# Optimization experiments

Measured on AMD Instinct MI355X. Metric: run time of the kernel, lower is better.

The kernel has to match this reference:

```python
import jax, jax.numpy as jnp
import numpy as np

D_MODEL = 2048
N_HEADS = 16
HEAD_DIM = D_MODEL // N_HEADS


def setup_inputs() -> dict:
    key = jax.random.key(0)
    ks = jax.random.split(key, 5)
    scale = 1.0 / np.sqrt(D_MODEL)
    x = jax.random.normal(ks[0], (2, 2048, D_MODEL), dtype=jnp.float32)
    W_qkv = jax.random.normal(ks[1], (D_MODEL, 3 * D_MODEL), dtype=jnp.float32) * scale
    b_qkv = jnp.zeros((3 * D_MODEL,), dtype=jnp.float32)
    W_out = jax.random.normal(ks[2], (D_MODEL, D_MODEL), dtype=jnp.float32) * scale
    b_out = jnp.zeros((D_MODEL,), dtype=jnp.float32)
    return {"x": x, "W_qkv": W_qkv, "b_qkv": b_qkv, "W_out": W_out, "b_out": b_out}


def reference(x, W_qkv, b_qkv, W_out, b_out):
    bsz, seq_len, _ = x.shape
    # QKV projection: (b, s, 3*d) -> (3, b, h, s, hd)
    qkv = x @ W_qkv + b_qkv
    qkv = qkv.reshape(bsz, seq_len, 3, N_HEADS, HEAD_DIM)
    qkv = jnp.transpose(qkv, (2, 0, 3, 1, 4))
    q, k, v = qkv[0], qkv[1], qkv[2]
    # scaled dot-product scores: (b, h, s, s)
    scores = jnp.einsum("bhqd,bhkd->bhqk", q, k) / np.sqrt(HEAD_DIM).astype(np.float32)
    causal = jnp.tril(jnp.ones((seq_len, seq_len), dtype=bool))
    scores = jnp.where(causal[None, None], scores, -jnp.inf)
    attn = jax.nn.softmax(scores, axis=-1)
    # attention output: (b, h, s, hd) -> (b, s, d)
    out = jnp.einsum("bhqk,bhkd->bhqd", attn, v)
    out = jnp.transpose(out, (0, 2, 1, 3)).reshape(bsz, seq_len, D_MODEL)
    y = out @ W_out + b_out
    return y
```

## Files before the change

kernel.cpp:

```cpp
#include <hip/hip_runtime.h>
#include <stdint.h>
#include <stddef.h>


typedef __attribute__((ext_vector_type(8))) short bf16x8;
typedef __attribute__((ext_vector_type(4))) float f32x4;

#define SOFT_SCALE 0.12751743075419806f

__device__ __forceinline__ short f2bf(float f) {
  union { float f; unsigned u; } v; v.f = f;
  unsigned u = v.u + 0x7fffu + ((v.u >> 16) & 1u);
  return (short)(u >> 16);
}

__device__ __forceinline__ void gload_lds16(const void* g, const void* l) {
  __builtin_amdgcn_global_load_lds(
      (__attribute__((address_space(1))) void*)(uintptr_t)g,
      (__attribute__((address_space(3))) void*)(uintptr_t)l,
      16, 0, 0);
}

__global__ __launch_bounds__(256) void cast_f32_bf16(
    const float* __restrict__ in, short* __restrict__ out, int n8) {
  int i = blockIdx.x * 256 + threadIdx.x;
  if (i >= n8) return;
  float4 a = ((const float4*)in)[i * 2];
  float4 b = ((const float4*)in)[i * 2 + 1];
  bf16x8 o;
  o[0] = f2bf(a.x); o[1] = f2bf(a.y); o[2] = f2bf(a.z); o[3] = f2bf(a.w);
  o[4] = f2bf(b.x); o[5] = f2bf(b.y); o[6] = f2bf(b.z); o[7] = f2bf(b.w);
  ((bf16x8*)out)[i] = o;
}

__global__ __launch_bounds__(256) void transpose_cast_w(
    const float* __restrict__ W, short* __restrict__ WT, int K, int N) {
  __shared__ short t[32][33];
  int k0 = blockIdx.x * 32, n0 = blockIdx.y * 32;
  int r = threadIdx.x >> 3;
  int c = (threadIdx.x & 7) * 4;
  float4 v = *(const float4*)(W + (size_t)(k0 + r) * N + n0 + c);
  t[r][c + 0] = f2bf(v.x); t[r][c + 1] = f2bf(v.y);
  t[r][c + 2] = f2bf(v.z); t[r][c + 3] = f2bf(v.w);
  __syncthreads();
  short4 o;
  o.x = t[c + 0][r]; o.y = t[c + 1][r]; o.z = t[c + 2][r]; o.w = t[c + 3][r];
  *(short4*)(WT + (size_t)(n0 + r) * K + k0 + c) = o;
}

template <int BF16OUT, int VTRANS, int QSCALE>
__global__ __launch_bounds__(256) void gemm_bt(
    const short* __restrict__ A, const short* __restrict__ BT,
    void* __restrict__ Cv, const float* __restrict__ bias,
    short* __restrict__ vTout, int M, int N, int K) {
  __shared__ __align__(16) short As[128 * 64];
  __shared__ __align__(16) short Bs[128 * 64];
  const int tid = threadIdx.x;
  const int wave = tid >> 6, lane = tid & 63;
  const int quad = lane >> 4, l16 = lane & 15;
  const int wmg = (wave >> 1) * 4;
  const int wng = (wave & 1) * 4;
  const int m0 = blockIdx.x * 128, n0 = blockIdx.y * 128;
  const int srow = lane >> 2;
  const int scol = (lane & 3) * 8;

  const short* aptr[4];
  const short* bptr[4];
#pragma unroll
  for (int it = 0; it < 4; ++it) {
    int c = wave * 4 + it;
    int row = (c >> 1) * 16 + srow, col = (c & 1) * 32 + scol;
    aptr[it] = A + (size_t)(m0 + row) * K + col;
    bptr[it] = BT + (size_t)(n0 + row) * K + col;
  }

  f32x4 acc[4][4] = {};

  for (int k0 = 0; k0 < K; k0 += 64) {
    __syncthreads();
#pragma unroll
    for (int it = 0; it < 4; ++it)
      gload_lds16(aptr[it], (const char*)As + (wave * 4 + it) * 1024);
#pragma unroll
    for (int it = 0; it < 4; ++it)
      gload_lds16(bptr[it], (const char*)Bs + (wave * 4 + it) * 1024);
#pragma unroll
    for (int it = 0; it < 4; ++it) { aptr[it] += 64; bptr[it] += 64; }
    __syncthreads();
#pragma unroll
    for (int kk = 0; kk < 2; ++kk) {
      bf16x8 af[4], bfg[4];
#pragma unroll
      for (int t = 0; t < 4; ++t)
        af[t] = *(const bf16x8*)(As + ((wmg + t) * 2 + kk) * 512 + l16 * 32 +
                                 quad * 8);
#pragma unroll
      for (int t = 0; t < 4; ++t)
        bfg[t] = *(const bf16x8*)(Bs + ((wng + t) * 2 + kk) * 512 + l16 * 32 +
                                  quad * 8);
#pragma unroll
      for (int tm = 0; tm < 4; ++tm)
#pragma unroll
        for (int tn = 0; tn < 4; ++tn)
          acc[tm][tn] = __builtin_amdgcn_mfma_f32_16x16x32_bf16(
              af[tm], bfg[tn], acc[tm][tn], 0, 0, 0);
    }
  }

  if (VTRANS && n0 >= 4096) {
#pragma unroll
    for (int tn = 0; tn < 4; ++tn) {
      int n = n0 + (wng + tn) * 16 + l16;
      float bv = bias[n];
      int hd = n - 4096;
#pragma unroll
      for (int tm = 0; tm < 4; ++tm) {
        int mb = m0 + (wmg + tm) * 16 + quad * 4;
        int bb = mb >> 11, s = mb & 2047;
        short4 o;
        o.x = f2bf(acc[tm][tn][0] + bv);
        o.y = f2bf(acc[tm][tn][1] + bv);
        o.z = f2bf(acc[tm][tn][2] + bv);
        o.w = f2bf(acc[tm][tn][3] + bv);
        *(short4*)(vTout + ((size_t)(bb * 2048 + hd)) * 2048 + s) = o;
      }
    }
    return;
  }

#pragma unroll
  for (int tn = 0; tn < 4; ++tn) {
    int n = n0 + (wng + tn) * 16 + l16;
    float bv = bias[n];
#pragma unroll
    for (int tm = 0; tm < 4; ++tm) {
      int mb = m0 + (wmg + tm) * 16 + quad * 4;
#pragma unroll
      for (int r = 0; r < 4; ++r) {
        float v = acc[tm][tn][r] + bv;
        if (QSCALE && n < 2048) v *= SOFT_SCALE;
        if (BF16OUT)
          ((short*)Cv)[(size_t)(mb + r) * N + n] = f2bf(v);
        else
          ((float*)Cv)[(size_t)(mb + r) * N + n] = v;
      }
    }
  }
}

__global__ __launch_bounds__(512, 4) void attn_kernel(
    const short* __restrict__ qkv, const short* __restrict__ vT,
    short* __restrict__ obuf) {
  __shared__ __align__(16) short Ks[32 * 512];
  __shared__ __align__(16) short Vs[32 * 512];
  const int tid = threadIdx.x;
  const int wave = tid >> 6, lane = tid & 63;
  const int quad = lane >> 4, l16 = lane & 15;
  const int bh = blockIdx.y, b = bh >> 4, h = bh & 15;
  const int px = blockIdx.x;
  const int p = (blockIdx.y & 16) ? (15 - px) : px;
  const int q0 = p * 128;
  const int nkt = p + 1;

  const short* qbase = qkv + (size_t)b * 2048 * 6144 + h * 128;
  const short* kbase = qkv + (size_t)b * 2048 * 6144 + 2048 + h * 128;
  const short* vtbase = vT + (size_t)bh * 128 * 2048;
  short* obase = obuf + (size_t)b * 2048 * 2048 + h * 128;

  const int srow = lane >> 2;
  const int scol = (lane & 3) * 8;

  bf16x8 ones;
#pragma unroll
  for (int j = 0; j < 8; ++j) ones[j] = (short)0x3F80;

  bf16x8 qf[4];
#pragma unroll
  for (int kk = 0; kk < 4; ++kk)
    qf[kk] = *(const bf16x8*)(
        qbase + (size_t)(q0 + wave * 16 + l16) * 6144 + kk * 32 + quad * 8);

  f32x4 acco[8] = {};
  f32x4 accl = {};

  for (int kt = 0; kt < nkt; ++kt) {
    const int k0 = kt * 128;
    __syncthreads();
#pragma unroll
    for (int it = 0; it < 4; ++it) {
      int c = wave * 4 + it;
      gload_lds16(
          kbase + (size_t)(k0 + (c & 7) * 16 + srow) * 6144 + (c >> 3) * 32 +
              scol,
          (const char*)Ks + c * 1024);
    }
#pragma unroll
    for (int it = 0; it < 4; ++it) {
      int c = wave * 4 + it;
      gload_lds16(
          vtbase + (size_t)((c & 7) * 16 + srow) * 2048 + k0 + (c >> 3) * 32 +
              scol,
          (const char*)Vs + c * 1024);
    }
    __syncthreads();

    f32x4 accs[8] = {};
#pragma unroll
    for (int kk = 0; kk < 4; ++kk) {
      bf16x8 bfg[8];
#pragma unroll
      for (int tn = 0; tn < 8; ++tn)
        bfg[tn] = *(const bf16x8*)(Ks + (kk * 8 + tn) * 512 + l16 * 32 +
                                   quad * 8);
#pragma unroll
      for (int tn = 0; tn < 8; ++tn)
        accs[tn] = __builtin_amdgcn_mfma_f32_16x16x32_bf16(
            qf[kk], bfg[tn], accs[tn], 0, 0, 0);
    }

    const bool diag = (kt == nkt - 1);
    if (diag) {
#pragma unroll
      for (int tn = 0; tn < 8; ++tn)
#pragma unroll
        for (int r = 0; r < 4; ++r) {
          int grow = q0 + wave * 16 + quad * 4 + r;
          int gcol = k0 + tn * 16 + l16;
          if (gcol > grow) accs[tn][r] = -1e30f;
        }
    }
#pragma unroll
    for (int tn = 0; tn < 8; ++tn)
#pragma unroll
      for (int r = 0; r < 4; ++r) accs[tn][r] = exp2f(accs[tn][r]);

    __syncthreads();

#pragma unroll
    for (int r = 0; r < 4; ++r) {
#pragma unroll
      for (int tn = 0; tn < 8; ++tn)
        Ks[(wave * 4 + (tn >> 1)) * 512 + (quad * 4 + r) * 32 + (tn & 1) * 16 +
           l16] = f2bf(accs[tn][r]);
    }

#pragma unroll
    for (int kk = 0; kk < 4; ++kk) {
      bf16x8 av = *(const bf16x8*)(Ks + (wave * 4 + kk) * 512 + l16 * 32 +
                                   quad * 8);
      accl = __builtin_amdgcn_mfma_f32_16x16x32_bf16(av, ones, accl, 0, 0, 0);
      bf16x8 bfg[8];
#pragma unroll
      for (int tn = 0; tn < 8; ++tn)
        bfg[tn] = *(const bf16x8*)(Vs + (kk * 8 + tn) * 512 + l16 * 32 +
                                   quad * 8);
#pragma unroll
      for (int tn = 0; tn < 8; ++tn)
        acco[tn] = __builtin_amdgcn_mfma_f32_16x16x32_bf16(
            av, bfg[tn], acco[tn], 0, 0, 0);
    }
  }

  float inv[4];
#pragma unroll
  for (int r = 0; r < 4; ++r) inv[r] = 1.f / accl[r];
#pragma unroll
  for (int r = 0; r < 4; ++r) {
    int row = q0 + wave * 16 + quad * 4 + r;
#pragma unroll
    for (int tn = 0; tn < 8; ++tn)
      obase[(size_t)row * 2048 + tn * 16 + l16] = f2bf(acco[tn][r] * inv[r]);
  }
}

extern "C" void kernel_launch(void* const* d_in, const int* in_sizes, int n_in,
                              void* d_out, int out_size, void* d_ws,
                              size_t ws_size, hipStream_t stream) {
  (void)in_sizes; (void)n_in; (void)out_size; (void)ws_size;
  const float* x    = (const float*)d_in[0];
  const float* Wqkv = (const float*)d_in[1];
  const float* bqkv = (const float*)d_in[2];
  const float* Wout = (const float*)d_in[3];
  const float* bout = (const float*)d_in[4];
  float* out = (float*)d_out;

  char* ws = (char*)d_ws;
  short* xb    = (short*)(ws);
  short* wqkvT = (short*)(ws + 16777216);
  short* woutT = (short*)(ws + 41943040);
  short* qkv   = (short*)(ws + 50331648);
  short* vTb   = (short*)(ws + 100663296);
  short* obuf  = (short*)(ws + 117440512);

  cast_f32_bf16<<<4096, 256, 0, stream>>>(x, xb, 1048576);
  transpose_cast_w<<<dim3(64, 192), 256, 0, stream>>>(Wqkv, wqkvT, 2048, 6144);
  transpose_cast_w<<<dim3(64, 64), 256, 0, stream>>>(Wout, woutT, 2048, 2048);

  gemm_bt<1, 1, 1><<<dim3(32, 48), 256, 0, stream>>>(
      xb, wqkvT, (void*)qkv, bqkv, vTb, 4096, 6144, 2048);

  attn_kernel<<<dim3(16, 32), 512, 0, stream>>>(qkv, vTb, obuf);

  gemm_bt<0, 0, 0><<<dim3(32, 16), 256, 0, stream>>>(
      obuf, woutT, (void*)out, bout, nullptr, 4096, 2048, 2048);
}
```

Measured before the change: 388.3 us.

## Double-buffer attention K/V tiles at 64-key granularity and stage V-transpose through LDS

The attention loop now works on 64-key tiles with two LDS buffers for K and V, so the next tile's global-to-LDS loads are issued while the current tile is computed. P is written to a separate Ps buffer, which removes one barrier per iteration. Separately, the V-transpose epilogue of the QKV GEMM stages results in padded shared memory and writes coalesced 16-byte rows instead of scattered short4 stores. The trade-offs are more LDS per attention block, which can lower occupancy, and twice as many loop iterations, each with less work.

```diff
diff --git a/kernel.cpp b/kernel.cpp
--- a/kernel.cpp
+++ b/kernel.cpp
@@ -53,8 +53,9 @@
     const short* __restrict__ A, const short* __restrict__ BT,
     void* __restrict__ Cv, const float* __restrict__ bias,
     short* __restrict__ vTout, int M, int N, int K) {
-  __shared__ __align__(16) short As[128 * 64];
-  __shared__ __align__(16) short Bs[128 * 64];
+  __shared__ __align__(16) short SH[128 * 136];
+  short* As = SH;
+  short* Bs = SH + 8192;
   const int tid = threadIdx.x;
   const int wave = tid >> 6, lane = tid & 63;
   const int quad = lane >> 4, l16 = lane & 15;
@@ -108,22 +109,28 @@
   }
 
   if (VTRANS && n0 >= 4096) {
+    __syncthreads();
 #pragma unroll
     for (int tn = 0; tn < 4; ++tn) {
-      int n = n0 + (wng + tn) * 16 + l16;
-      float bv = bias[n];
-      int hd = n - 4096;
+      int hd = (wng + tn) * 16 + l16;
+      float bv = bias[n0 + hd];
 #pragma unroll
       for (int tm = 0; tm < 4; ++tm) {
-        int mb = m0 + (wmg + tm) * 16 + quad * 4;
-        int bb = mb >> 11, s = mb & 2047;
-        short4 o;
-        o.x = f2bf(acc[tm][tn][0] + bv);
-        o.y = f2bf(acc[tm][tn][1] + bv);
-        o.z = f2bf(acc[tm][tn][2] + bv);
-        o.w = f2bf(acc[tm][tn][3] + bv);
-        *(short4*)(vTout + ((size_t)(bb * 2048 + hd)) * 2048 + s) = o;
+        int sl = (wmg + tm) * 16 + quad * 4;
+#pragma unroll
+        for (int r = 0; r < 4; ++r)
+          SH[hd * 136 + sl + r] = f2bf(acc[tm][tn][r] + bv);
       }
+    }
+    __syncthreads();
+    const int bb = m0 >> 11, s0 = m0 & 2047, hd0 = n0 - 4096;
+#pragma unroll
+    for (int pass = 0; pass < 8; ++pass) {
+      int row = pass * 16 + (tid >> 4);
+      int c16 = (tid & 15) * 8;
+      bf16x8 v = *(const bf16x8*)(SH + row * 136 + c16);
+      *(bf16x8*)(vTout + ((size_t)(bb * 2048 + hd0 + row)) * 2048 + s0 + c16) =
+          v;
     }
     return;
   }
@@ -151,8 +158,9 @@
 __global__ __launch_bounds__(512, 4) void attn_kernel(
     const short* __restrict__ qkv, const short* __restrict__ vT,
     short* __restrict__ obuf) {
-  __shared__ __align__(16) short Ks[32 * 512];
-  __shared__ __align__(16) short Vs[32 * 512];
+  __shared__ __align__(16) short Ks[2 * 8192];
+  __shared__ __align__(16) short Vs[2 * 8192];
+  __shared__ __align__(16) short Ps[8192];
   const int tid = threadIdx.x;
   const int wave = tid >> 6, lane = tid & 63;
   const int quad = lane >> 4, l16 = lane & 15;
@@ -160,7 +168,7 @@
   const int px = blockIdx.x;
   const int p = (blockIdx.y & 16) ? (15 - px) : px;
   const int q0 = p * 128;
-  const int nkt = p + 1;
+  const int nkt = 2 * (p + 1);
 
   const short* qbase = qkv + (size_t)b * 2048 * 6144 + h * 128;
   const short* kbase = qkv + (size_t)b * 2048 * 6144 + 2048 + h * 128;
@@ -183,45 +191,53 @@
   f32x4 acco[8] = {};
   f32x4 accl = {};
 
-  for (int kt = 0; kt < nkt; ++kt) {
-    const int k0 = kt * 128;
-    __syncthreads();
-#pragma unroll
-    for (int it = 0; it < 4; ++it) {
-      int c = wave * 4 + it;
+  auto stage = [&](int buf, int kt) {
+    const int k0 = kt * 64;
+#pragma unroll
+    for (int it = 0; it < 2; ++it) {
+      int c = wave * 2 + it;
       gload_lds16(
-          kbase + (size_t)(k0 + (c & 7) * 16 + srow) * 6144 + (c >> 3) * 32 +
+          kbase + (size_t)(k0 + (c & 3) * 16 + srow) * 6144 + (c >> 2) * 32 +
               scol,
-          (const char*)Ks + c * 1024);
-    }
-#pragma unroll
-    for (int it = 0; it < 4; ++it) {
-      int c = wave * 4 + it;
+          (const char*)Ks + buf * 16384 + c * 1024);
+    }
+#pragma unroll
+    for (int it = 0; it < 2; ++it) {
+      int c = wave * 2 + it;
       gload_lds16(
           vtbase + (size_t)((c & 7) * 16 + srow) * 2048 + k0 + (c >> 3) * 32 +
               scol,
-          (const char*)Vs + c * 1024);
-    }
-    __syncthreads();
-
-    f32x4 accs[8] = {};
+          (const char*)Vs + buf * 16384 + c * 1024);
+    }
+  };
+
+  stage(0, 0);
+
+  for (int kt = 0; kt < nkt; ++kt) {
+    const int buf = kt & 1;
+    __syncthreads();
+    if (kt + 1 < nkt) stage(1 - buf, kt + 1);
+    const short* KsB = Ks + buf * 8192;
+    const short* VsB = Vs + buf * 8192;
+
+    f32x4 accs[4] = {};
 #pragma unroll
     for (int kk = 0; kk < 4; ++kk) {
-      bf16x8 bfg[8];
-#pragma unroll
-      for (int tn = 0; tn < 8; ++tn)
-        bfg[tn] = *(const bf16x8*)(Ks + (kk * 8 + tn) * 512 + l16 * 32 +
+      bf16x8 bfg[4];
+#pragma unroll
+      for (int tn = 0; tn < 4; ++tn)
+        bfg[tn] = *(const bf16x8*)(KsB + (kk * 4 + tn) * 512 + l16 * 32 +
                                    quad * 8);
 #pragma unroll
-      for (int tn = 0; tn < 8; ++tn)
+      for (int tn = 0; tn < 4; ++tn)
         accs[tn] = __builtin_amdgcn_mfma_f32_16x16x32_bf16(
             qf[kk], bfg[tn], accs[tn], 0, 0, 0);
     }
 
-    const bool diag = (kt == nkt - 1);
-    if (diag) {
-#pragma unroll
-      for (int tn = 0; tn < 8; ++tn)
+    if (kt >= nkt - 2) {
+      const int k0 = kt * 64;
+#pragma unroll
+      for (int tn = 0; tn < 4; ++tn)
 #pragma unroll
         for (int r = 0; r < 4; ++r) {
           int grow = q0 + wave * 16 + quad * 4 + r;
@@ -230,29 +246,26 @@
         }
     }
 #pragma unroll
-    for (int tn = 0; tn < 8; ++tn)
+    for (int tn = 0; tn < 4; ++tn)
 #pragma unroll
       for (int r = 0; r < 4; ++r) accs[tn][r] = exp2f(accs[tn][r]);
 
-    __syncthreads();
-
-#pragma unroll
-    for (int r = 0; r < 4; ++r) {
-#pragma unroll
-      for (int tn = 0; tn < 8; ++tn)
-        Ks[(wave * 4 + (tn >> 1)) * 512 + (quad * 4 + r) * 32 + (tn & 1) * 16 +
-           l16] = f2bf(accs[tn][r]);
-    }
-
-#pragma unroll
-    for (int kk = 0; kk < 4; ++kk) {
-      bf16x8 av = *(const bf16x8*)(Ks + (wave * 4 + kk) * 512 + l16 * 32 +
+#pragma unroll
+    for (int r = 0; r < 4; ++r)
+#pragma unroll
+      for (int tn = 0; tn < 4; ++tn)
+        Ps[wave * 1024 + (tn >> 1) * 512 + (quad * 4 + r) * 32 +
+           (tn & 1) * 16 + l16] = f2bf(accs[tn][r]);
+
+#pragma unroll
+    for (int kk2 = 0; kk2 < 2; ++kk2) {
+      bf16x8 av = *(const bf16x8*)(Ps + wave * 1024 + kk2 * 512 + l16 * 32 +
                                    quad * 8);
       accl = __builtin_amdgcn_mfma_f32_16x16x32_bf16(av, ones, accl, 0, 0, 0);
       bf16x8 bfg[8];
 #pragma unroll
       for (int tn = 0; tn < 8; ++tn)
-        bfg[tn] = *(const bf16x8*)(Vs + (kk * 8 + tn) * 512 + l16 * 32 +
+        bfg[tn] = *(const bf16x8*)(VsB + (kk2 * 8 + tn) * 512 + l16 * 32 +
                                    quad * 8);
 #pragma unroll
       for (int tn = 0; tn < 8; ++tn)
```

Result: faster. 368.2 us (-5.2%).
